# Optimization experiments

Hardware: AMD Instinct MI355X
Metric: run time of the kernel (lower is better)

## Reference

```python
import jax, jax.numpy as jnp
import numpy as np

B, SEQ, D, N_LAYERS, HEADS, D_FF = 256, 43, 18, 6, 3, 2048
A_MAX, NB = 128, 7
EPS = 1e-6


def _norm(x, a, b):
    mu = x.mean(-1, keepdims=True)
    sd = jnp.std(x, axis=-1, ddof=1, keepdims=True)  # torch std is unbiased
    return a * (x - mu) / (sd + EPS) + b


def _attn(x, Wq, bq, Wk, bk, Wv, bv, Wo, bo, mask):
    b_, s, d = x.shape
    dk = d // HEADS
    def split_heads(W, bb):
        return (x @ W + bb).reshape(b_, s, HEADS, dk).transpose(0, 2, 1, 3)
    q, k, v = split_heads(Wq, bq), split_heads(Wk, bk), split_heads(Wv, bv)
    scores = jnp.einsum('bhqd,bhkd->bhqk', q, k) / jnp.sqrt(jnp.float32(dk))
    scores = jnp.where(mask[:, None, :, :] == 0, -1e9, scores)  # mask [B,1,S] -> [B,1,1,S]
    attn = jax.nn.softmax(scores, axis=-1)
    o = jnp.einsum('bhqk,bhkd->bhqd', attn, v).transpose(0, 2, 1, 3).reshape(b_, s, d)
    return o @ Wo + bo


def setup_inputs() -> dict:
    key = jax.random.key(0)
    ks = iter(jax.random.split(key, 40))
    g = lambda shape, s=0.05: jax.random.normal(next(ks), shape, dtype=jnp.float32) * s
    inp = {
        'src': jax.random.normal(next(ks), (B, SEQ, D), dtype=jnp.float32),
        'mask': jnp.ones((B, 1, SEQ), dtype=jnp.int32),
        'max_atoms': A_MAX,
        'enc_Wq': g((N_LAYERS, D, D)), 'enc_bq': g((N_LAYERS, D)),
        'enc_Wk': g((N_LAYERS, D, D)), 'enc_bk': g((N_LAYERS, D)),
        'enc_Wv': g((N_LAYERS, D, D)), 'enc_bv': g((N_LAYERS, D)),
        'enc_Wo': g((N_LAYERS, D, D)), 'enc_bo': g((N_LAYERS, D)),
        'enc_ln1_a': jnp.ones((N_LAYERS, D), jnp.float32), 'enc_ln1_b': jnp.zeros((N_LAYERS, D), jnp.float32),
        'enc_ln2_a': jnp.ones((N_LAYERS, D), jnp.float32), 'enc_ln2_b': jnp.zeros((N_LAYERS, D), jnp.float32),
        'enc_ffW1': g((N_LAYERS, D, D_FF)), 'enc_ffb1': g((N_LAYERS, D_FF)),
        'enc_ffW2': g((N_LAYERS, D_FF, D)), 'enc_ffb2': g((N_LAYERS, D)),
        'll2_W': g((D, A_MAX)), 'll2_b': g((A_MAX,)),
        'll_W': g((SEQ, A_MAX)), 'll_b': g((A_MAX,)),
        'fl_W': g((2 * A_MAX, NB)), 'fl_b': g((NB,)),
    }
    return inp


def reference(src, enc_Wq, enc_bq, enc_Wk, enc_bk, enc_Wv, enc_bv, enc_Wo, enc_bo,
              enc_ln1_a, enc_ln1_b, enc_ln2_a, enc_ln2_b,
              enc_ffW1, enc_ffb1, enc_ffW2, enc_ffb2,
              ll2_W, ll2_b, ll_W, ll_b, fl_W, fl_b, mask, max_atoms):
    # --- Encoder (dropout=0 at eval; no final norm, as in source) ---
    x = src
    for i in range(N_LAYERS):
        x2 = _norm(x, enc_ln1_a[i], enc_ln1_b[i])
        x = x + _attn(x2, enc_Wq[i], enc_bq[i], enc_Wk[i], enc_bk[i],
                      enc_Wv[i], enc_bv[i], enc_Wo[i], enc_bo[i], mask)
        x2 = _norm(x, enc_ln2_a[i], enc_ln2_b[i])
        x = x + (jax.nn.relu(x2 @ enc_ffW1[i] + enc_ffb1[i]) @ enc_ffW2[i] + enc_ffb2[i])
    # --- EdgeClassify2 ---
    red = x @ ll2_W + ll2_b            # [B, S, A]
    red = red.transpose(0, 2, 1)       # [B, A, S]
    R = red @ ll_W + ll_b              # [B, A, A]; repeat_e[:,i,i,:] == R[:,i,:]
    # final_e[b,i,j] = concat(R[b,i], R[b,j]); fl(concat) = R_i@W1 + R_j@W2 + b (exact)
    W1, W2 = fl_W[:max_atoms], fl_W[max_atoms:]
    P = R @ W1                          # [B, A, nb]
    Q = R @ W2                          # [B, A, nb]
    return P[:, :, None, :] + Q[:, None, :, :] + fl_b  # [B, A, A, nb]
```

## Files before the change

kernel.cpp:

```cpp
#include <hip/hip_runtime.h>
#include <math.h>

namespace {

constexpr int Sq = 43;
constexpr int Dm = 18;
constexpr int Dff = 2048;
constexpr int Am = 128;
constexpr int Nb = 7;
constexpr int NR = 11008;
constexpr int RSZ = NR * Dm;
constexpr int WROW = 20;
constexpr float EPSf = 1e-6f;

typedef float v2f __attribute__((ext_vector_type(2)));
typedef float v4f __attribute__((ext_vector_type(4)));

__global__ __launch_bounds__(64) void k_attn(
    int layer,
    const float* __restrict__ Xi, float* __restrict__ Xn,
    float* __restrict__ x2g,
    const int* __restrict__ maskg,
    const float* __restrict__ Wq, const float* __restrict__ bq,
    const float* __restrict__ Wk, const float* __restrict__ bk,
    const float* __restrict__ Wv, const float* __restrict__ bv,
    const float* __restrict__ ln1a, const float* __restrict__ ln1b,
    const float* __restrict__ Wo, const float* __restrict__ bo,
    const float* __restrict__ ln2a, const float* __restrict__ ln2b,
    const float* __restrict__ b2g,
    const float* __restrict__ fW1g, const float* __restrict__ fb1g,
    const float* __restrict__ fW2g,
    float* __restrict__ W1P, float* __restrict__ W2P,
    const float* __restrict__ llW, const float* __restrict__ llb,
    const float* __restrict__ flW, const float* __restrict__ flb,
    const float* __restrict__ ll2b,
    float* __restrict__ Mw, float* __restrict__ PS1, float* __restrict__ QS2)
{
    __shared__ __align__(16) float ks[Sq * 20];
    __shared__ __align__(16) float vs[Sq * 20];
    __shared__ int ms[Sq];
    __shared__ float M[602];
    __shared__ float cc2[14];
    __shared__ float SS[14];

    const int tid = threadIdx.x;
    const int b = blockIdx.x;

    if (b >= 256) {
        if (b < 448) {
            const int idx = (b - 256) * 64 + tid;
            const int l = idx / Dff;
            const int j = idx - l * Dff;
            float* o1 = W1P + (size_t)idx * WROW;
            float* o2 = W2P + (size_t)idx * WROW;
            #pragma unroll
            for (int d = 0; d < Dm; d++)
                o1[d] = fW1g[(size_t)l * Dm * Dff + (size_t)d * Dff + j];
            o1[18] = fb1g[l * Dff + j];
            o1[19] = 0.f;
            #pragma unroll
            for (int d = 0; d < Dm; d++)
                o2[d] = fW2g[((size_t)l * Dff + j) * Dm + d];
            o2[18] = 0.f;
            o2[19] = 0.f;
            if (idx < WROW) {
                W1P[(size_t)6 * Dff * WROW + idx] = 0.f;
                W2P[(size_t)6 * Dff * WROW + idx] = 0.f;
            }
            return;
        }
        for (int m = tid; m < 602; m += 64) {
            int half = m / 301, rem = m - half * 301;
            int s = rem / 7, n = rem - 7 * s;
            float a = 0.f;
            for (int jj = 0; jj < Am; jj++)
                a += llW[s * Am + jj] * flW[(half * Am + jj) * Nb + n];
            M[m] = a;
        }
        if (tid < 14) {
            int half = tid / 7, n = tid - 7 * (tid / 7);
            float a = 0.f;
            for (int jj = 0; jj < Am; jj++)
                a += llb[jj] * flW[(half * Am + jj) * Nb + n];
            cc2[tid] = a;
        }
        __syncthreads();
        if (tid < 14) {
            int half = tid / 7, n = tid - 7 * (tid / 7);
            float s2 = 0.f;
            for (int s = 0; s < Sq; s++) s2 += M[half * 301 + s * 7 + n];
            SS[tid] = s2;
        }
        __syncthreads();
        for (int m = tid; m < 602; m += 64) Mw[m] = M[m];
        for (int m = tid; m < 896; m += 64) {
            int i = m / 7, n = m - 7 * i;
            PS1[m] = cc2[n] + ll2b[i] * SS[n];
            QS2[m] = cc2[7 + n] + ll2b[i] * SS[7 + n] + flb[n];
        }
        return;
    }

    const float scale = 0.40824829046386296f;

    if (tid < Sq) ms[tid] = maskg[b * Sq + tid];

    float y[Dm];
    float qv[Dm];
    if (tid < Sq) {
        const size_t ro = (size_t)(b * Sq + tid) * Dm;
        #pragma unroll
        for (int k = 0; k < 9; k++) {
            float2 t = *(const float2*)(Xi + ro + 2 * k);
            y[2 * k] = t.x; y[2 * k + 1] = t.y;
        }
        float mu = 0.f;
        #pragma unroll
        for (int d = 0; d < Dm; d++) mu += y[d];
        mu *= (1.f / Dm);
        float var = 0.f;
        #pragma unroll
        for (int d = 0; d < Dm; d++) { float t = y[d] - mu; var += t * t; }
        var *= (1.f / (Dm - 1));
        float isd = 1.f / (sqrtf(var) + EPSf);
        float x2[Dm];
        #pragma unroll
        for (int d = 0; d < Dm; d++)
            x2[d] = ln1a[layer * Dm + d] * (y[d] - mu) * isd
                  + ln1b[layer * Dm + d];
        const float* wqp = Wq + layer * Dm * Dm;
        const float* wkp = Wk + layer * Dm * Dm;
        const float* wvp = Wv + layer * Dm * Dm;
        #pragma unroll 3
        for (int d = 0; d < Dm; d++) {
            float aq = bq[layer * Dm + d];
            float ak = bk[layer * Dm + d];
            float av = bv[layer * Dm + d];
            #pragma unroll
            for (int dd = 0; dd < Dm; dd++) {
                aq += x2[dd] * wqp[dd * Dm + d];
                ak += x2[dd] * wkp[dd * Dm + d];
                av += x2[dd] * wvp[dd * Dm + d];
            }
            qv[d] = aq;
            ks[tid * 20 + d] = ak;
            vs[tid * 20 + d] = av;
        }
    }
    __syncthreads();
    if (tid >= Sq) return;

    float o[Dm];
    #pragma unroll
    for (int h = 0; h < 3; h++) {
        float sum = 0.f;
        float o6[6];
        #pragma unroll
        for (int d = 0; d < 6; d++) o6[d] = 0.f;
        const float q0 = qv[h * 6], q1 = qv[h * 6 + 1], q2 = qv[h * 6 + 2];
        const float q3 = qv[h * 6 + 3], q4 = qv[h * 6 + 4], q5 = qv[h * 6 + 5];
        for (int j = 0; j < Sq; j++) {
            const float* kr = ks + j * 20 + h * 6;
            const float2 k0 = *(const float2*)(kr);
            const float2 k1 = *(const float2*)(kr + 2);
            const float2 k2 = *(const float2*)(kr + 4);
            float t = q0 * k0.x + q1 * k0.y + q2 * k1.x +
                      q3 * k1.y + q4 * k2.x + q5 * k2.y;
            t *= scale;
            if (ms[j] == 0) t = -1e9f;
            float e = __expf(t);
            sum += e;
            const float* vr = vs + j * 20 + h * 6;
            const float2 v0 = *(const float2*)(vr);
            const float2 v1 = *(const float2*)(vr + 2);
            const float2 v2 = *(const float2*)(vr + 4);
            o6[0] += e * v0.x; o6[1] += e * v0.y; o6[2] += e * v1.x;
            o6[3] += e * v1.y; o6[4] += e * v2.x; o6[5] += e * v2.y;
        }
        float inv = 1.f / sum;
        #pragma unroll
        for (int d = 0; d < 6; d++) o[h * 6 + d] = o6[d] * inv;
    }

    const float* wo = Wo + layer * Dm * Dm;
    float yo[Dm];
    #pragma unroll 3
    for (int d = 0; d < Dm; d++) {
        float t = bo[layer * Dm + d];
        #pragma unroll
        for (int dd = 0; dd < Dm; dd++) t += o[dd] * wo[dd * Dm + d];
        yo[d] = y[d] + t;
    }
    const size_t ro = (size_t)(b * Sq + tid) * Dm;
    #pragma unroll
    for (int d = 0; d < Dm; d++)
        Xn[ro + d] = yo[d] + b2g[layer * Dm + d];
    float mu = 0.f;
    #pragma unroll
    for (int d = 0; d < Dm; d++) mu += yo[d];
    mu *= (1.f / Dm);
    float var = 0.f;
    #pragma unroll
    for (int d = 0; d < Dm; d++) { float t = yo[d] - mu; var += t * t; }
    var *= (1.f / (Dm - 1));
    float isd = 1.f / (sqrtf(var) + EPSf);
    #pragma unroll
    for (int d = 0; d < Dm; d++)
        x2g[ro + d] =
            ln2a[layer * Dm + d] * (yo[d] - mu) * isd + ln2b[layer * Dm + d];
}

__global__ __launch_bounds__(256, 3) void k_ffn(
    int layer, const float* __restrict__ x2g,
    const float* __restrict__ W1P, const float* __restrict__ W2P,
    float* __restrict__ Xn)
{
    __shared__ float Ls[4 * 64 * Dm];

    const int tid  = threadIdx.x;
    const int lane = tid & 63;
    const int wv   = __builtin_amdgcn_readfirstlane(tid >> 6);
    const int rg   = blockIdx.x >> 3;
    const int q    = blockIdx.x & 7;
    const int row  = rg * 64 + lane;
    const int j0   = q * 256 + wv * 64;

    const v4f* w1p = (const v4f*)(W1P + ((size_t)layer * Dff + j0) * WROW);
    const v4f* w2p = (const v4f*)(W2P + ((size_t)layer * Dff + j0) * WROW);

    v2f xp[9];
    #pragma unroll
    for (int k = 0; k < 9; k++)
        xp[k] = *(const v2f*)(x2g + (size_t)row * Dm + 2 * k);

    v2f acc2[9];
    #pragma unroll
    for (int k = 0; k < 9; k++) acc2[k] = (v2f){0.f, 0.f};

    v4f a0 = w1p[0], a1 = w1p[1], a2 = w1p[2], a3 = w1p[3], a4 = w1p[4];
    v4f c0 = w2p[0], c1 = w2p[1], c2 = w2p[2], c3 = w2p[3], c4 = w2p[4];

    for (int jj = 0; jj < 64; jj++) {
        const v4f* n1 = w1p + (jj + 1) * 5;
        const v4f* n2 = w2p + (jj + 1) * 5;
        const v4f na0 = n1[0], na1 = n1[1], na2 = n1[2], na3 = n1[3], na4 = n1[4];
        const v4f nc0 = n2[0], nc1 = n2[1], nc2 = n2[2], nc3 = n2[3], nc4 = n2[4];

        v2f h2 = xp[0] * a0.lo;
        h2 = __builtin_elementwise_fma(xp[1], a0.hi, h2);
        h2 = __builtin_elementwise_fma(xp[2], a1.lo, h2);
        h2 = __builtin_elementwise_fma(xp[3], a1.hi, h2);
        h2 = __builtin_elementwise_fma(xp[4], a2.lo, h2);
        h2 = __builtin_elementwise_fma(xp[5], a2.hi, h2);
        h2 = __builtin_elementwise_fma(xp[6], a3.lo, h2);
        h2 = __builtin_elementwise_fma(xp[7], a3.hi, h2);
        h2 = __builtin_elementwise_fma(xp[8], a4.lo, h2);
        float h = a4.z + h2.x + h2.y;
        h = fmaxf(h, 0.f);
        const v2f hh = {h, h};

        acc2[0] = __builtin_elementwise_fma(hh, c0.lo, acc2[0]);
        acc2[1] = __builtin_elementwise_fma(hh, c0.hi, acc2[1]);
        acc2[2] = __builtin_elementwise_fma(hh, c1.lo, acc2[2]);
        acc2[3] = __builtin_elementwise_fma(hh, c1.hi, acc2[3]);
        acc2[4] = __builtin_elementwise_fma(hh, c2.lo, acc2[4]);
        acc2[5] = __builtin_elementwise_fma(hh, c2.hi, acc2[5]);
        acc2[6] = __builtin_elementwise_fma(hh, c3.lo, acc2[6]);
        acc2[7] = __builtin_elementwise_fma(hh, c3.hi, acc2[7]);
        acc2[8] = __builtin_elementwise_fma(hh, c4.lo, acc2[8]);

        a0 = na0; a1 = na1; a2 = na2; a3 = na3; a4 = na4;
        c0 = nc0; c1 = nc1; c2 = nc2; c3 = nc3; c4 = nc4;
    }

    #pragma unroll
    for (int k = 0; k < 9; k++) {
        Ls[(wv * 64 + lane) * Dm + 2 * k]     = acc2[k].x;
        Ls[(wv * 64 + lane) * Dm + 2 * k + 1] = acc2[k].y;
    }
    __syncthreads();
    for (int e = tid; e < 1152; e += 256) {
        float s = Ls[e] + Ls[1152 + e] + Ls[2304 + e] + Ls[3456 + e];
        unsafeAtomicAdd(&Xn[(size_t)rg * 1152 + e], s);
    }
}

__global__ __launch_bounds__(256) void k_out(
    const float* __restrict__ xg,
    const float* __restrict__ ll2W,
    const float* __restrict__ Mw, const float* __restrict__ PS1,
    const float* __restrict__ QS2, float* __restrict__ out)
{
    __shared__ float xb[Sq * Dm];
    __shared__ float M[602];
    __shared__ float T[2][Dm][Nb];
    __shared__ float Pc[32 * Nb];
    __shared__ float QBs[Am * Nb];

    const int b = blockIdx.y, chunk = blockIdx.x, tid = threadIdx.x;

    for (int e = tid; e < Sq * Dm; e += 256)
        xb[e] = xg[(size_t)b * (Sq * Dm) + e];
    for (int m = tid; m < 602; m += 256) M[m] = Mw[m];
    __syncthreads();

    for (int m = tid; m < 252; m += 256) {
        int half = m / 126, rem = m - half * 126;
        int d = rem / 7, n = rem - 7 * d;
        float a = 0.f;
        for (int s = 0; s < Sq; s++)
            a += xb[s * Dm + d] * M[half * 301 + s * 7 + n];
        T[half][d][n] = a;
    }
    __syncthreads();

    for (int m = tid; m < 224; m += 256) {
        int il = m / 7, n = m - 7 * il;
        int i = chunk * 32 + il;
        float a = PS1[i * 7 + n];
        #pragma unroll
        for (int d = 0; d < Dm; d++) a += T[0][d][n] * ll2W[d * Am + i];
        Pc[m] = a;
    }
    for (int e = tid; e < 896; e += 256) {
        int jj = e / 7, n = e - 7 * jj;
        float a = QS2[e];
        #pragma unroll
        for (int d = 0; d < Dm; d++) a += T[1][d][n] * ll2W[d * Am + jj];
        QBs[e] = a;
    }
    __syncthreads();

    if (tid < 224) {
        const int e = 4 * tid;
        const float q0 = QBs[e], q1 = QBs[e + 1], q2 = QBs[e + 2], q3 = QBs[e + 3];
        const int n0 = e % 7, n1 = (e + 1) % 7, n2 = (e + 2) % 7, n3 = (e + 3) % 7;
        const size_t base = (size_t)b * (Am * Am * Nb)
                          + (size_t)chunk * 32 * 896 + e;
        for (int il = 0; il < 32; il++) {
            const float* pc = Pc + il * 7;
            float4 v;
            v.x = pc[n0] + q0; v.y = pc[n1] + q1;
            v.z = pc[n2] + q2; v.w = pc[n3] + q3;
            *(float4*)(out + base + (size_t)il * 896) = v;
        }
    }
}

}

extern "C" void kernel_launch(void* const* d_in, const int* in_sizes, int n_in,
                              void* d_out, int out_size, void* d_ws, size_t ws_size,
                              hipStream_t stream)
{
    (void)in_sizes; (void)n_in; (void)out_size; (void)ws_size;

    const float* src  = (const float*)d_in[0];
    const int*   mask = (const int*)  d_in[1];
    const float* Wq   = (const float*)d_in[3];
    const float* bq   = (const float*)d_in[4];
    const float* Wk   = (const float*)d_in[5];
    const float* bk   = (const float*)d_in[6];
    const float* Wv   = (const float*)d_in[7];
    const float* bv   = (const float*)d_in[8];
    const float* Wo   = (const float*)d_in[9];
    const float* bo   = (const float*)d_in[10];
    const float* ln1a = (const float*)d_in[11];
    const float* ln1b = (const float*)d_in[12];
    const float* ln2a = (const float*)d_in[13];
    const float* ln2b = (const float*)d_in[14];
    const float* fW1  = (const float*)d_in[15];
    const float* fb1  = (const float*)d_in[16];
    const float* fW2  = (const float*)d_in[17];
    const float* fb2  = (const float*)d_in[18];
    const float* ll2W = (const float*)d_in[19];
    const float* ll2b = (const float*)d_in[20];
    const float* llW  = (const float*)d_in[21];
    const float* llb  = (const float*)d_in[22];
    const float* flW  = (const float*)d_in[23];
    const float* flb  = (const float*)d_in[24];
    float* out = (float*)d_out;

    const size_t WPSZ = (size_t)6 * Dff * WROW + WROW;

    float* ws  = (float*)d_ws;
    float* xA  = ws;
    float* xB  = ws + 1 * (size_t)RSZ;
    float* x2g = ws + 2 * (size_t)RSZ;
    float* W1P = ws + 3 * (size_t)RSZ;
    float* W2P = W1P + WPSZ;
    float* Mw  = W2P + WPSZ;
    float* PS1 = Mw + 604;
    float* QS2 = PS1 + 896;

    for (int i = 0; i < 6; i++) {
        const float* Xi = (i == 0) ? src : ((i % 2 == 1) ? xB : xA);
        float*       Xn = (i % 2 == 0) ? xB : xA;
        const int nblk = (i == 0) ? 449 : 256;
        k_attn<<<nblk, 64, 0, stream>>>(i, Xi, Xn, x2g, mask,
                                        Wq, bq, Wk, bk, Wv, bv,
                                        ln1a, ln1b, Wo, bo, ln2a, ln2b, fb2,
                                        fW1, fb1, fW2, W1P, W2P,
                                        llW, llb, flW, flb, ll2b,
                                        Mw, PS1, QS2);
        k_ffn<<<1376, 256, 0, stream>>>(i, x2g, W1P, W2P, Xn);
    }
    k_out<<<dim3(4, 256), 256, 0, stream>>>(xA, ll2W, Mw, PS1, QS2, out);
}
```

Baseline: 510.8 us.

## Stage per-wave FFN weight slices in LDS and raise k_ffn occupancy

```diff
diff --git a/kernel.cpp b/kernel.cpp
--- a/kernel.cpp
+++ b/kernel.cpp
@@ -210,12 +210,12 @@
             ln2a[layer * Dm + d] * (yo[d] - mu) * isd + ln2b[layer * Dm + d];
 }
 
-__global__ __launch_bounds__(256, 3) void k_ffn(
+__global__ __launch_bounds__(256, 4) void k_ffn(
     int layer, const float* __restrict__ x2g,
     const float* __restrict__ W1P, const float* __restrict__ W2P,
     float* __restrict__ Xn)
 {
-    __shared__ float Ls[4 * 64 * Dm];
+    __shared__ __align__(16) float wbuf[10240];
 
     const int tid  = threadIdx.x;
     const int lane = tid & 63;
@@ -225,8 +225,16 @@
     const int row  = rg * 64 + lane;
     const int j0   = q * 256 + wv * 64;
 
-    const v4f* w1p = (const v4f*)(W1P + ((size_t)layer * Dff + j0) * WROW);
-    const v4f* w2p = (const v4f*)(W2P + ((size_t)layer * Dff + j0) * WROW);
+    {
+        const v4f* g1 = (const v4f*)(W1P + ((size_t)layer * Dff + j0) * WROW);
+        const v4f* g2 = (const v4f*)(W2P + ((size_t)layer * Dff + j0) * WROW);
+        v4f* s1 = (v4f*)(wbuf + wv * 2560);
+        v4f* s2 = (v4f*)(wbuf + wv * 2560 + 1280);
+        #pragma unroll
+        for (int k = 0; k < 5; k++) s1[64 * k + lane] = g1[64 * k + lane];
+        #pragma unroll
+        for (int k = 0; k < 5; k++) s2[64 * k + lane] = g2[64 * k + lane];
+    }
 
     v2f xp[9];
     #pragma unroll
@@ -237,14 +245,15 @@
     #pragma unroll
     for (int k = 0; k < 9; k++) acc2[k] = (v2f){0.f, 0.f};
 
-    v4f a0 = w1p[0], a1 = w1p[1], a2 = w1p[2], a3 = w1p[3], a4 = w1p[4];
-    v4f c0 = w2p[0], c1 = w2p[1], c2 = w2p[2], c3 = w2p[3], c4 = w2p[4];
-
+    const float* wb1 = wbuf + wv * 2560;
+    const float* wb2 = wbuf + wv * 2560 + 1280;
+
+    #pragma unroll 2
     for (int jj = 0; jj < 64; jj++) {
-        const v4f* n1 = w1p + (jj + 1) * 5;
-        const v4f* n2 = w2p + (jj + 1) * 5;
-        const v4f na0 = n1[0], na1 = n1[1], na2 = n1[2], na3 = n1[3], na4 = n1[4];
-        const v4f nc0 = n2[0], nc1 = n2[1], nc2 = n2[2], nc3 = n2[3], nc4 = n2[4];
+        const v4f* w1r = (const v4f*)(wb1 + jj * 20);
+        const v4f* w2r = (const v4f*)(wb2 + jj * 20);
+        const v4f a0 = w1r[0], a1 = w1r[1], a2 = w1r[2], a3 = w1r[3], a4 = w1r[4];
+        const v4f c0 = w2r[0], c1 = w2r[1], c2 = w2r[2], c3 = w2r[3], c4 = w2r[4];
 
         v2f h2 = xp[0] * a0.lo;
         h2 = __builtin_elementwise_fma(xp[1], a0.hi, h2);
@@ -268,19 +277,17 @@
         acc2[6] = __builtin_elementwise_fma(hh, c3.lo, acc2[6]);
         acc2[7] = __builtin_elementwise_fma(hh, c3.hi, acc2[7]);
         acc2[8] = __builtin_elementwise_fma(hh, c4.lo, acc2[8]);
-
-        a0 = na0; a1 = na1; a2 = na2; a3 = na3; a4 = na4;
-        c0 = nc0; c1 = nc1; c2 = nc2; c3 = nc3; c4 = nc4;
-    }
-
+    }
+
+    __syncthreads();
     #pragma unroll
     for (int k = 0; k < 9; k++) {
-        Ls[(wv * 64 + lane) * Dm + 2 * k]     = acc2[k].x;
-        Ls[(wv * 64 + lane) * Dm + 2 * k + 1] = acc2[k].y;
+        wbuf[(wv * 64 + lane) * Dm + 2 * k]     = acc2[k].x;
+        wbuf[(wv * 64 + lane) * Dm + 2 * k + 1] = acc2[k].y;
     }
     __syncthreads();
     for (int e = tid; e < 1152; e += 256) {
-        float s = Ls[e] + Ls[1152 + e] + Ls[2304 + e] + Ls[3456 + e];
+        float s = wbuf[e] + wbuf[1152 + e] + wbuf[2304 + e] + wbuf[3456 + e];
         unsafeAtomicAdd(&Xn[(size_t)rg * 1152 + e], s);
     }
 }
```

New measurement: 559.3 us. 1.1x slower.

## Split attention kernel across three per-head wavefronts per batch block

Applied to the files above, without the earlier changes.

```diff
diff --git a/kernel.cpp b/kernel.cpp
--- a/kernel.cpp
+++ b/kernel.cpp
@@ -16,7 +16,7 @@
 typedef float v2f __attribute__((ext_vector_type(2)));
 typedef float v4f __attribute__((ext_vector_type(4)));
 
-__global__ __launch_bounds__(64) void k_attn(
+__global__ __launch_bounds__(192) void k_attn(
     int layer,
     const float* __restrict__ Xi, float* __restrict__ Xn,
     float* __restrict__ x2g,
@@ -38,6 +38,7 @@
 {
     __shared__ __align__(16) float ks[Sq * 20];
     __shared__ __align__(16) float vs[Sq * 20];
+    __shared__ float os[Sq * Dm];
     __shared__ int ms[Sq];
     __shared__ float M[602];
     __shared__ float cc2[14];
@@ -47,8 +48,8 @@
     const int b = blockIdx.x;
 
     if (b >= 256) {
-        if (b < 448) {
-            const int idx = (b - 256) * 64 + tid;
+        if (b < 320) {
+            const int idx = (b - 256) * 192 + tid;
             const int l = idx / Dff;
             const int j = idx - l * Dff;
             float* o1 = W1P + (size_t)idx * WROW;
@@ -69,7 +70,7 @@
             }
             return;
         }
-        for (int m = tid; m < 602; m += 64) {
+        for (int m = tid; m < 602; m += 192) {
             int half = m / 301, rem = m - half * 301;
             int s = rem / 7, n = rem - 7 * s;
             float a = 0.f;
@@ -92,8 +93,8 @@
             SS[tid] = s2;
         }
         __syncthreads();
-        for (int m = tid; m < 602; m += 64) Mw[m] = M[m];
-        for (int m = tid; m < 896; m += 64) {
+        for (int m = tid; m < 602; m += 192) Mw[m] = M[m];
+        for (int m = tid; m < 896; m += 192) {
             int i = m / 7, n = m - 7 * i;
             PS1[m] = cc2[n] + ll2b[i] * SS[n];
             QS2[m] = cc2[7 + n] + ll2b[i] * SS[7 + n] + flb[n];
@@ -102,13 +103,15 @@
     }
 
     const float scale = 0.40824829046386296f;
+    const int h = tid >> 6;
+    const int q = tid & 63;
 
     if (tid < Sq) ms[tid] = maskg[b * Sq + tid];
 
     float y[Dm];
-    float qv[Dm];
-    if (tid < Sq) {
-        const size_t ro = (size_t)(b * Sq + tid) * Dm;
+    float qv6[6];
+    if (q < Sq) {
+        const size_t ro = (size_t)(b * Sq + q) * Dm;
         #pragma unroll
         for (int k = 0; k < 9; k++) {
             float2 t = *(const float2*)(Xi + ro + 2 * k);
@@ -131,8 +134,9 @@
         const float* wqp = Wq + layer * Dm * Dm;
         const float* wkp = Wk + layer * Dm * Dm;
         const float* wvp = Wv + layer * Dm * Dm;
-        #pragma unroll 3
-        for (int d = 0; d < Dm; d++) {
+        #pragma unroll
+        for (int dh = 0; dh < 6; dh++) {
+            const int d = h * 6 + dh;
             float aq = bq[layer * Dm + d];
             float ak = bk[layer * Dm + d];
             float av = bv[layer * Dm + d];
@@ -142,23 +146,20 @@
                 ak += x2[dd] * wkp[dd * Dm + d];
                 av += x2[dd] * wvp[dd * Dm + d];
             }
-            qv[d] = aq;
-            ks[tid * 20 + d] = ak;
-            vs[tid * 20 + d] = av;
-        }
-    }
-    __syncthreads();
-    if (tid >= Sq) return;
-
-    float o[Dm];
-    #pragma unroll
-    for (int h = 0; h < 3; h++) {
+            qv6[dh] = aq;
+            ks[q * 20 + d] = ak;
+            vs[q * 20 + d] = av;
+        }
+    }
+    __syncthreads();
+
+    if (q < Sq) {
         float sum = 0.f;
         float o6[6];
         #pragma unroll
         for (int d = 0; d < 6; d++) o6[d] = 0.f;
-        const float q0 = qv[h * 6], q1 = qv[h * 6 + 1], q2 = qv[h * 6 + 2];
-        const float q3 = qv[h * 6 + 3], q4 = qv[h * 6 + 4], q5 = qv[h * 6 + 5];
+        const float q0 = qv6[0], q1 = qv6[1], q2 = qv6[2];
+        const float q3 = qv6[3], q4 = qv6[4], q5 = qv6[5];
         for (int j = 0; j < Sq; j++) {
             const float* kr = ks + j * 20 + h * 6;
             const float2 k0 = *(const float2*)(kr);
@@ -179,35 +180,39 @@
         }
         float inv = 1.f / sum;
         #pragma unroll
-        for (int d = 0; d < 6; d++) o[h * 6 + d] = o6[d] * inv;
-    }
-
-    const float* wo = Wo + layer * Dm * Dm;
-    float yo[Dm];
-    #pragma unroll 3
-    for (int d = 0; d < Dm; d++) {
-        float t = bo[layer * Dm + d];
-        #pragma unroll
-        for (int dd = 0; dd < Dm; dd++) t += o[dd] * wo[dd * Dm + d];
-        yo[d] = y[d] + t;
-    }
-    const size_t ro = (size_t)(b * Sq + tid) * Dm;
-    #pragma unroll
-    for (int d = 0; d < Dm; d++)
-        Xn[ro + d] = yo[d] + b2g[layer * Dm + d];
-    float mu = 0.f;
-    #pragma unroll
-    for (int d = 0; d < Dm; d++) mu += yo[d];
-    mu *= (1.f / Dm);
-    float var = 0.f;
-    #pragma unroll
-    for (int d = 0; d < Dm; d++) { float t = yo[d] - mu; var += t * t; }
-    var *= (1.f / (Dm - 1));
-    float isd = 1.f / (sqrtf(var) + EPSf);
-    #pragma unroll
-    for (int d = 0; d < Dm; d++)
-        x2g[ro + d] =
-            ln2a[layer * Dm + d] * (yo[d] - mu) * isd + ln2b[layer * Dm + d];
+        for (int d = 0; d < 6; d++) os[q * Dm + h * 6 + d] = o6[d] * inv;
+    }
+    __syncthreads();
+
+    if (h == 0 && q < Sq) {
+        const float* wo = Wo + layer * Dm * Dm;
+        const float* orow = os + q * Dm;
+        float yo[Dm];
+        #pragma unroll 3
+        for (int d = 0; d < Dm; d++) {
+            float t = bo[layer * Dm + d];
+            #pragma unroll
+            for (int dd = 0; dd < Dm; dd++) t += orow[dd] * wo[dd * Dm + d];
+            yo[d] = y[d] + t;
+        }
+        const size_t ro = (size_t)(b * Sq + q) * Dm;
+        #pragma unroll
+        for (int d = 0; d < Dm; d++)
+            Xn[ro + d] = yo[d] + b2g[layer * Dm + d];
+        float mu = 0.f;
+        #pragma unroll
+        for (int d = 0; d < Dm; d++) mu += yo[d];
+        mu *= (1.f / Dm);
+        float var = 0.f;
+        #pragma unroll
+        for (int d = 0; d < Dm; d++) { float t = yo[d] - mu; var += t * t; }
+        var *= (1.f / (Dm - 1));
+        float isd = 1.f / (sqrtf(var) + EPSf);
+        #pragma unroll
+        for (int d = 0; d < Dm; d++)
+            x2g[ro + d] =
+                ln2a[layer * Dm + d] * (yo[d] - mu) * isd + ln2b[layer * Dm + d];
+    }
 }
 
 __global__ __launch_bounds__(256, 3) void k_ffn(
@@ -396,13 +401,13 @@
     for (int i = 0; i < 6; i++) {
         const float* Xi = (i == 0) ? src : ((i % 2 == 1) ? xB : xA);
         float*       Xn = (i % 2 == 0) ? xB : xA;
-        const int nblk = (i == 0) ? 449 : 256;
-        k_attn<<<nblk, 64, 0, stream>>>(i, Xi, Xn, x2g, mask,
-                                        Wq, bq, Wk, bk, Wv, bv,
-                                        ln1a, ln1b, Wo, bo, ln2a, ln2b, fb2,
-                                        fW1, fb1, fW2, W1P, W2P,
-                                        llW, llb, flW, flb, ll2b,
-                                        Mw, PS1, QS2);
+        const int nblk = (i == 0) ? 321 : 256;
+        k_attn<<<nblk, 192, 0, stream>>>(i, Xi, Xn, x2g, mask,
+                                         Wq, bq, Wk, bk, Wv, bv,
+                                         ln1a, ln1b, Wo, bo, ln2a, ln2b, fb2,
+                                         fW1, fb1, fW2, W1P, W2P,
+                                         llW, llb, flW, flb, ll2b,
+                                         Mw, PS1, QS2);
         k_ffn<<<1376, 256, 0, stream>>>(i, x2g, W1P, W2P, Xn);
     }
     k_out<<<dim3(4, 256), 256, 0, stream>>>(xA, ll2W, Mw, PS1, QS2, out);
```

Result: faster. 484.3 us (-5.2%).
